# Performance work log

Hardware: AMD Instinct MI355X
Metric: run time of the kernel (lower is better)

The kernel has to match this reference:

```python
import jax, jax.numpy as jnp
import numpy as np

NEG_SLOPE = 0.2  # LeakyReLU slope from the torch module


def setup_inputs() -> dict:
    key = jax.random.key(0)
    k1, k2, k3 = jax.random.split(key, 3)
    B, N, IN = 32, 512, 256
    H, D = 8, 32  # out_dim=256, concat=True -> head_dim = 256 // 8
    x = jax.random.normal(k1, (B, N, IN), dtype=jnp.float32)
    # nn.Linear(in_dim, H*D, bias=False).weight has shape (H*D, in_dim)
    W = jax.random.normal(k2, (H * D, IN), dtype=jnp.float32) * (1.0 / np.sqrt(IN))
    # xavier_uniform on (1, H, 2D)
    limit = float(np.sqrt(6.0 / (H + 2 * D)))
    attn = jax.random.uniform(k3, (1, H, 2 * D), dtype=jnp.float32, minval=-limit, maxval=limit)
    return {"x": x, "W": W, "attn": attn}


def reference(x, W, attn):
    # x: (B, N, IN); W: (H*D, IN); attn: (1, H, 2D)
    B, N, _ = x.shape
    H = attn.shape[1]
    D = attn.shape[2] // 2
    Wx = (x @ W.T).reshape(B, N, H, D)  # (B, N, H, D)
    # Additive attention decomposes: e[b,i,j,h] = leaky(s_src[b,i,h] + s_tgt[b,j,h]).
    # (src = Wx broadcast over j, tgt = Wx broadcast over i; cat*attn sums split in two.)
    a_src = attn[0, :, :D]  # (H, D)
    a_tgt = attn[0, :, D:]  # (H, D)
    s_src = jnp.einsum('bnhd,hd->bnh', Wx, a_src)
    s_tgt = jnp.einsum('bnhd,hd->bnh', Wx, a_tgt)
    e = jax.nn.leaky_relu(s_src[:, :, None, :] + s_tgt[:, None, :, :], NEG_SLOPE)  # (B,N,N,H)
    a = jax.nn.softmax(e, axis=2)  # softmax over source nodes j
    # dropout p=0 (eval mode) -> identity
    out = jnp.einsum('bijh,bjhd->bihd', a, Wx)  # (B, N, H, D)
    out = out.reshape(B, N, H * D)  # concat=True
    return jax.nn.elu(out)
```

## Files before the change

kernel.cpp:

```cpp
#include <hip/hip_runtime.h>
#include <math.h>

#define NEG_SLOPE 0.2f
#define LOG2E 1.44269504088896f

typedef _Float16 f16x8 __attribute__((ext_vector_type(8)));
typedef float f32x4 __attribute__((ext_vector_type(4)));

union PK8 { uint4 u4; _Float16 h[8]; };
union PK4 { uint2 u2; _Float16 h[4]; };
union PK1 { unsigned short u; _Float16 h; };

__global__ __launch_bounds__(256) void gemm_wxt(const float* __restrict__ x,
                                                const float* __restrict__ W,
                                                unsigned short* __restrict__ wxtg) {
    __shared__ __align__(16) unsigned short xs[64 * 64];
    __shared__ __align__(16) unsigned short pool[128 * 64];
    unsigned short* ws = pool;
    unsigned short* tb = pool;

    const int tid = threadIdx.x;
    const int bid = blockIdx.x;
    const int m0 = (bid >> 1) * 64;
    const int n0 = (bid & 1) * 128;
    const int w = tid >> 6, l = tid & 63;
    const int q = l >> 4, ln = l & 15;
    const int iw = (w & 1) * 32, nw = (w >> 1) * 64;

    f32x4 acc[2][4];
    #pragma unroll
    for (int g = 0; g < 2; ++g)
        #pragma unroll
        for (int t = 0; t < 4; ++t) acc[g][t] = (f32x4){0.f, 0.f, 0.f, 0.f};

    for (int kc = 0; kc < 256; kc += 64) {
        __syncthreads();
        {
            const int i = tid >> 2, kq = tid & 3;
            const float* src = x + (size_t)(m0 + i) * 256 + kc + kq * 16;
            float4 v0 = *(const float4*)(src + 0);
            float4 v1 = *(const float4*)(src + 4);
            float4 v2 = *(const float4*)(src + 8);
            float4 v3 = *(const float4*)(src + 12);
            PK8 p0, p1;
            p0.h[0] = (_Float16)v0.x; p0.h[1] = (_Float16)v0.y;
            p0.h[2] = (_Float16)v0.z; p0.h[3] = (_Float16)v0.w;
            p0.h[4] = (_Float16)v1.x; p0.h[5] = (_Float16)v1.y;
            p0.h[6] = (_Float16)v1.z; p0.h[7] = (_Float16)v1.w;
            p1.h[0] = (_Float16)v2.x; p1.h[1] = (_Float16)v2.y;
            p1.h[2] = (_Float16)v2.z; p1.h[3] = (_Float16)v2.w;
            p1.h[4] = (_Float16)v3.x; p1.h[5] = (_Float16)v3.y;
            p1.h[6] = (_Float16)v3.z; p1.h[7] = (_Float16)v3.w;
            int b0 = i * 128 + kq * 32;
            *(uint4*)((char*)xs + (b0 ^ ((i & 7) << 4))) = p0.u4;
            *(uint4*)((char*)xs + ((b0 + 16) ^ ((i & 7) << 4))) = p1.u4;
        }
        {
            const int kq = tid & 15, nr = tid >> 4;
            #pragma unroll
            for (int p = 0; p < 8; ++p) {
                int n = p * 16 + nr;
                float4 v = *(const float4*)(W + (size_t)(n0 + n) * 256 + kc + kq * 4);
                PK4 pk;
                pk.h[0] = (_Float16)v.x; pk.h[1] = (_Float16)v.y;
                pk.h[2] = (_Float16)v.z; pk.h[3] = (_Float16)v.w;
                *(uint2*)((char*)ws + ((n * 128 + kq * 8) ^ ((n & 7) << 4))) = pk.u2;
            }
        }
        __syncthreads();

        #pragma unroll
        for (int ks = 0; ks < 2; ++ks) {
            const int kb = ks * 64 + q * 16;
            f16x8 af[2];
            #pragma unroll
            for (int g = 0; g < 2; ++g) {
                int row = iw + g * 16 + ln;
                uint4 raw = *(const uint4*)((const char*)xs +
                            ((row * 128 + kb) ^ ((row & 7) << 4)));
                PK8 pk; pk.u4 = raw;
                af[g] = *(f16x8*)&pk;
            }
            #pragma unroll
            for (int t = 0; t < 4; ++t) {
                int n = nw + t * 16 + ln;
                uint4 raw = *(const uint4*)((const char*)ws +
                            ((n * 128 + kb) ^ ((n & 7) << 4)));
                PK8 pk; pk.u4 = raw;
                f16x8 bf = *(f16x8*)&pk;
                acc[0][t] = __builtin_amdgcn_mfma_f32_16x16x32_f16(af[0], bf, acc[0][t], 0, 0, 0);
                acc[1][t] = __builtin_amdgcn_mfma_f32_16x16x32_f16(af[1], bf, acc[1][t], 0, 0, 0);
            }
        }
    }

    __syncthreads();
    #pragma unroll
    for (int g = 0; g < 2; ++g)
        #pragma unroll
        for (int t = 0; t < 4; ++t)
            #pragma unroll
            for (int r = 0; r < 4; ++r) {
                int n  = nw + t * 16 + ln;
                int jl = iw + g * 16 + q * 4 + r;
                PK1 hv; hv.h = (_Float16)acc[g][t][r];
                *(unsigned short*)((char*)tb + ((n * 128 + jl * 2) ^ ((n & 7) << 4))) = hv.u;
            }
    __syncthreads();
    {
        const int b = m0 >> 9, j0 = m0 & 511;
        #pragma unroll
        for (int p = 0; p < 4; ++p) {
            int idx = p * 256 + tid;
            int n = idx >> 3, c = idx & 7;
            uint4 v = *(const uint4*)((const char*)tb + ((n * 128 + c * 16) ^ ((n & 7) << 4)));
            int nn = n0 + n;
            *(uint4*)(wxtg + ((size_t)(b * 256 + nn) * 512 + j0 + c * 8)) = v;
        }
    }
}

__global__ __launch_bounds__(512) void gat_attn(const unsigned short* __restrict__ wxtg,
                                                const float* __restrict__ attn,
                                                float* __restrict__ out) {
    __shared__ __align__(16) unsigned short wxt[32 * 512];
    __shared__ float stf[512];
    __shared__ float ssrc[512];
    __shared__ float red_s[8];

    const int bid = blockIdx.x;
    const int bh = bid & 255, q4 = bid >> 8;
    const int b = bh >> 3, h = bh & 7;
    const int tid = threadIdx.x;
    const int w = tid >> 6, l = tid & 63;
    const int q = l >> 4, ln = l & 15;

    {
        const unsigned short* src = wxtg + (size_t)bh * 32 * 512;
        const int d = tid >> 4, cs = tid & 15;
        #pragma unroll
        for (int p = 0; p < 4; ++p) {
            int c = p * 16 + cs;
            uint4 v = *(const uint4*)(src + d * 512 + c * 8);
            *(uint4*)((char*)wxt + ((d * 1024 + c * 16) ^ ((d & 7) << 4))) = v;
        }
    }
    __syncthreads();

    {
        const int j = tid;
        float ss = 0.f, st = 0.f;
        #pragma unroll
        for (int d = 0; d < 32; ++d) {
            PK1 hv;
            hv.u = *(const unsigned short*)((const char*)wxt +
                    ((d * 1024 + j * 2) ^ ((d & 7) << 4)));
            float v = (float)hv.h;
            ss += v * attn[h * 64 + d];
            st += v * attn[h * 64 + 32 + d];
        }
        ssrc[j] = ss * LOG2E;
        float stv = st * LOG2E;
        stf[j] = stv;
        float m = stv;
        #pragma unroll
        for (int off = 32; off > 0; off >>= 1)
            m = fmaxf(m, __shfl_xor(m, off));
        if (l == 0) red_s[w] = m;
    }
    __syncthreads();
    float maxtK = red_s[0];
    #pragma unroll
    for (int ww = 1; ww < 8; ++ww) maxtK = fmaxf(maxtK, red_s[ww]);

    const int ibase = q4 * 128 + w * 16;
    float ciK, miK;
    {
        float cc = ssrc[ibase + ln];
        float cm = cc + maxtK;
        miK = fmaxf(cm, NEG_SLOPE * cm);
        ciK = cc;
    }

    f32x4 acc0 = (f32x4){0.f, 0.f, 0.f, 0.f};
    f32x4 acc1 = (f32x4){0.f, 0.f, 0.f, 0.f};
    float pd = 0.f;

    for (int kk = 0; kk < 16; ++kk) {
        const int j0 = kk * 32 + q * 8;
        float4 s0 = *(const float4*)(stf + j0);
        float4 s1 = *(const float4*)(stf + j0 + 4);
        float st[8] = {s0.x, s0.y, s0.z, s0.w, s1.x, s1.y, s1.z, s1.w};

        f16x8 bf[2];
        #pragma unroll
        for (int dt = 0; dt < 2; ++dt) {
            int d = dt * 16 + ln;
            int bb = d * 1024 + kk * 64 + q * 16;
            uint4 raw = *(const uint4*)((const char*)wxt + (bb ^ ((d & 7) << 4)));
            PK8 pk; pk.u4 = raw;
            bf[dt] = *(f16x8*)&pk;
        }

        f16x8 pa;
        float s = 0.f;
        #pragma unroll
        for (int e = 0; e < 8; ++e) {
            float eK = ciK + st[e];
            float lr = fmaxf(eK, NEG_SLOPE * eK);
            float p = exp2f(lr - miK);
            s += p;
            pa[e] = (_Float16)p;
        }
        pd += s;
        acc0 = __builtin_amdgcn_mfma_f32_16x16x32_f16(pa, bf[0], acc0, 0, 0, 0);
        acc1 = __builtin_amdgcn_mfma_f32_16x16x32_f16(pa, bf[1], acc1, 0, 0, 0);
    }

    pd += __shfl_xor(pd, 16);
    pd += __shfl_xor(pd, 32);
    float inv = 1.f / pd;

    #pragma unroll
    for (int dt = 0; dt < 2; ++dt) {
        f32x4 a = dt ? acc1 : acc0;
        #pragma unroll
        for (int r = 0; r < 4; ++r) {
            int row = q * 4 + r;
            float dn = __shfl(inv, row);
            float o = a[r] * dn;
            o = o > 0.f ? o : (__expf(o) - 1.f);
            size_t i = (size_t)(b * 512 + ibase + row);
            out[i * 256 + h * 32 + dt * 16 + ln] = o;
        }
    }
}

extern "C" void kernel_launch(void* const* d_in, const int* in_sizes, int n_in,
                              void* d_out, int out_size, void* d_ws, size_t ws_size,
                              hipStream_t stream) {
    const float* x    = (const float*)d_in[0];
    const float* W    = (const float*)d_in[1];
    const float* attn = (const float*)d_in[2];
    float* out = (float*)d_out;

    unsigned short* wxtg = (unsigned short*)d_ws;

    gemm_wxt<<<512, 256, 0, stream>>>(x, W, wxtg);
    gat_attn<<<1024, 512, 0, stream>>>(wxtg, attn, out);
}
```

Before: 44.52 us.

## Pre-convert inputs to fp16, halve attention grid with two row groups per warp

Adds a separate kernel that converts x and W to fp16 in workspace, so the GEMM loads half-width data and W is no longer converted again by every block. The attention kernel now handles 32 rows per warp (two MFMA row groups) over 512 blocks instead of 1024. This halves the redundant per-block staging of Wx and the score computation, and it switches to the hardware exp2 builtin. The cost is an extra launch plus a full fp16 round trip of x through global memory, and fewer blocks with more registers per thread.

Result: faster. 39.24 us (-11.9%).

```diff
diff --git a/kernel.cpp b/kernel.cpp
--- a/kernel.cpp
+++ b/kernel.cpp
@@ -4,15 +4,49 @@
 #define NEG_SLOPE 0.2f
 #define LOG2E 1.44269504088896f
 
+#if __has_builtin(__builtin_amdgcn_exp2f)
+#define EXP2F __builtin_amdgcn_exp2f
+#else
+#define EXP2F exp2f
+#endif
+
 typedef _Float16 f16x8 __attribute__((ext_vector_type(8)));
 typedef float f32x4 __attribute__((ext_vector_type(4)));
 
 union PK8 { uint4 u4; _Float16 h[8]; };
-union PK4 { uint2 u2; _Float16 h[4]; };
 union PK1 { unsigned short u; _Float16 h; };
 
-__global__ __launch_bounds__(256) void gemm_wxt(const float* __restrict__ x,
-                                                const float* __restrict__ W,
+#define XN_CHUNKS (32 * 512 * 256 / 8)
+#define WN_CHUNKS (256 * 256 / 8)
+
+__global__ __launch_bounds__(256) void cvt_f16(const float* __restrict__ x,
+                                               const float* __restrict__ W,
+                                               unsigned short* __restrict__ xf,
+                                               unsigned short* __restrict__ wf) {
+    int idx = blockIdx.x * 256 + threadIdx.x;
+    const float* src;
+    unsigned short* dst;
+    if (idx < XN_CHUNKS) {
+        src = x + (size_t)idx * 8;
+        dst = xf + (size_t)idx * 8;
+    } else {
+        int j = idx - XN_CHUNKS;
+        if (j >= WN_CHUNKS) return;
+        src = W + (size_t)j * 8;
+        dst = wf + (size_t)j * 8;
+    }
+    float4 v0 = *(const float4*)(src);
+    float4 v1 = *(const float4*)(src + 4);
+    PK8 p;
+    p.h[0] = (_Float16)v0.x; p.h[1] = (_Float16)v0.y;
+    p.h[2] = (_Float16)v0.z; p.h[3] = (_Float16)v0.w;
+    p.h[4] = (_Float16)v1.x; p.h[5] = (_Float16)v1.y;
+    p.h[6] = (_Float16)v1.z; p.h[7] = (_Float16)v1.w;
+    *(uint4*)dst = p.u4;
+}
+
+__global__ __launch_bounds__(256) void gemm_wxt(const unsigned short* __restrict__ xf,
+                                                const unsigned short* __restrict__ wf,
                                                 unsigned short* __restrict__ wxtg) {
     __shared__ __align__(16) unsigned short xs[64 * 64];
     __shared__ __align__(16) unsigned short pool[128 * 64];
@@ -35,37 +69,19 @@
 
     for (int kc = 0; kc < 256; kc += 64) {
         __syncthreads();
-        {
-            const int i = tid >> 2, kq = tid & 3;
-            const float* src = x + (size_t)(m0 + i) * 256 + kc + kq * 16;
-            float4 v0 = *(const float4*)(src + 0);
-            float4 v1 = *(const float4*)(src + 4);
-            float4 v2 = *(const float4*)(src + 8);
-            float4 v3 = *(const float4*)(src + 12);
-            PK8 p0, p1;
-            p0.h[0] = (_Float16)v0.x; p0.h[1] = (_Float16)v0.y;
-            p0.h[2] = (_Float16)v0.z; p0.h[3] = (_Float16)v0.w;
-            p0.h[4] = (_Float16)v1.x; p0.h[5] = (_Float16)v1.y;
-            p0.h[6] = (_Float16)v1.z; p0.h[7] = (_Float16)v1.w;
-            p1.h[0] = (_Float16)v2.x; p1.h[1] = (_Float16)v2.y;
-            p1.h[2] = (_Float16)v2.z; p1.h[3] = (_Float16)v2.w;
-            p1.h[4] = (_Float16)v3.x; p1.h[5] = (_Float16)v3.y;
-            p1.h[6] = (_Float16)v3.z; p1.h[7] = (_Float16)v3.w;
-            int b0 = i * 128 + kq * 32;
-            *(uint4*)((char*)xs + (b0 ^ ((i & 7) << 4))) = p0.u4;
-            *(uint4*)((char*)xs + ((b0 + 16) ^ ((i & 7) << 4))) = p1.u4;
-        }
-        {
-            const int kq = tid & 15, nr = tid >> 4;
-            #pragma unroll
-            for (int p = 0; p < 8; ++p) {
-                int n = p * 16 + nr;
-                float4 v = *(const float4*)(W + (size_t)(n0 + n) * 256 + kc + kq * 4);
-                PK4 pk;
-                pk.h[0] = (_Float16)v.x; pk.h[1] = (_Float16)v.y;
-                pk.h[2] = (_Float16)v.z; pk.h[3] = (_Float16)v.w;
-                *(uint2*)((char*)ws + ((n * 128 + kq * 8) ^ ((n & 7) << 4))) = pk.u2;
-            }
+        #pragma unroll
+        for (int p = 0; p < 2; ++p) {
+            int idx = p * 256 + tid;
+            int row = idx >> 3, c = idx & 7;
+            uint4 v = *(const uint4*)(xf + (size_t)(m0 + row) * 256 + kc + c * 8);
+            *(uint4*)((char*)xs + ((row * 128 + c * 16) ^ ((row & 7) << 4))) = v;
+        }
+        #pragma unroll
+        for (int p = 0; p < 4; ++p) {
+            int idx = p * 256 + tid;
+            int n = idx >> 3, c = idx & 7;
+            uint4 v = *(const uint4*)(wf + (size_t)(n0 + n) * 256 + kc + c * 8);
+            *(uint4*)((char*)ws + ((n * 128 + c * 16) ^ ((n & 7) << 4))) = v;
         }
         __syncthreads();
 
@@ -120,16 +136,16 @@
     }
 }
 
-__global__ __launch_bounds__(512) void gat_attn(const unsigned short* __restrict__ wxtg,
-                                                const float* __restrict__ attn,
-                                                float* __restrict__ out) {
+__global__ __launch_bounds__(512, 4) void gat_attn(const unsigned short* __restrict__ wxtg,
+                                                   const float* __restrict__ attn,
+                                                   float* __restrict__ out) {
     __shared__ __align__(16) unsigned short wxt[32 * 512];
     __shared__ float stf[512];
     __shared__ float ssrc[512];
     __shared__ float red_s[8];
 
     const int bid = blockIdx.x;
-    const int bh = bid & 255, q4 = bid >> 8;
+    const int bh = bid & 255, half = bid >> 8;
     const int b = bh >> 3, h = bh & 7;
     const int tid = threadIdx.x;
     const int w = tid >> 6, l = tid & 63;
@@ -173,18 +189,23 @@
     #pragma unroll
     for (int ww = 1; ww < 8; ++ww) maxtK = fmaxf(maxtK, red_s[ww]);
 
-    const int ibase = q4 * 128 + w * 16;
-    float ciK, miK;
-    {
-        float cc = ssrc[ibase + ln];
+    const int ibase = half * 256 + w * 32;
+    float ciK[2], miK[2];
+    #pragma unroll
+    for (int g = 0; g < 2; ++g) {
+        float cc = ssrc[ibase + g * 16 + ln];
         float cm = cc + maxtK;
-        miK = fmaxf(cm, NEG_SLOPE * cm);
-        ciK = cc;
-    }
-
-    f32x4 acc0 = (f32x4){0.f, 0.f, 0.f, 0.f};
-    f32x4 acc1 = (f32x4){0.f, 0.f, 0.f, 0.f};
-    float pd = 0.f;
+        miK[g] = fmaxf(cm, NEG_SLOPE * cm);
+        ciK[g] = cc;
+    }
+
+    f32x4 acc[2][2];
+    #pragma unroll
+    for (int g = 0; g < 2; ++g) {
+        acc[g][0] = (f32x4){0.f, 0.f, 0.f, 0.f};
+        acc[g][1] = (f32x4){0.f, 0.f, 0.f, 0.f};
+    }
+    float pd[2] = {0.f, 0.f};
 
     for (int kk = 0; kk < 16; ++kk) {
         const int j0 = kk * 32 + q * 8;
@@ -202,38 +223,45 @@
             bf[dt] = *(f16x8*)&pk;
         }
 
-        f16x8 pa;
-        float s = 0.f;
-        #pragma unroll
-        for (int e = 0; e < 8; ++e) {
-            float eK = ciK + st[e];
-            float lr = fmaxf(eK, NEG_SLOPE * eK);
-            float p = exp2f(lr - miK);
-            s += p;
-            pa[e] = (_Float16)p;
-        }
-        pd += s;
-        acc0 = __builtin_amdgcn_mfma_f32_16x16x32_f16(pa, bf[0], acc0, 0, 0, 0);
-        acc1 = __builtin_amdgcn_mfma_f32_16x16x32_f16(pa, bf[1], acc1, 0, 0, 0);
-    }
-
-    pd += __shfl_xor(pd, 16);
-    pd += __shfl_xor(pd, 32);
-    float inv = 1.f / pd;
-
-    #pragma unroll
-    for (int dt = 0; dt < 2; ++dt) {
-        f32x4 a = dt ? acc1 : acc0;
-        #pragma unroll
-        for (int r = 0; r < 4; ++r) {
-            int row = q * 4 + r;
-            float dn = __shfl(inv, row);
-            float o = a[r] * dn;
-            o = o > 0.f ? o : (__expf(o) - 1.f);
-            size_t i = (size_t)(b * 512 + ibase + row);
-            out[i * 256 + h * 32 + dt * 16 + ln] = o;
-        }
-    }
+        #pragma unroll
+        for (int g = 0; g < 2; ++g) {
+            f16x8 pa;
+            float s = 0.f;
+            #pragma unroll
+            for (int e = 0; e < 8; ++e) {
+                float eK = ciK[g] + st[e];
+                float lr = fmaxf(eK, NEG_SLOPE * eK);
+                float p = EXP2F(lr - miK[g]);
+                s += p;
+                pa[e] = (_Float16)p;
+            }
+            pd[g] += s;
+            acc[g][0] = __builtin_amdgcn_mfma_f32_16x16x32_f16(pa, bf[0], acc[g][0], 0, 0, 0);
+            acc[g][1] = __builtin_amdgcn_mfma_f32_16x16x32_f16(pa, bf[1], acc[g][1], 0, 0, 0);
+        }
+    }
+
+    float inv[2];
+    #pragma unroll
+    for (int g = 0; g < 2; ++g) {
+        float s = pd[g];
+        s += __shfl_xor(s, 16);
+        s += __shfl_xor(s, 32);
+        inv[g] = 1.f / s;
+    }
+    #pragma unroll
+    for (int g = 0; g < 2; ++g)
+        #pragma unroll
+        for (int dt = 0; dt < 2; ++dt)
+            #pragma unroll
+            for (int r = 0; r < 4; ++r) {
+                int row = q * 4 + r;
+                float dn = __shfl(inv[g], row);
+                float o = acc[g][dt][r] * dn;
+                o = o > 0.f ? o : (__expf(o) - 1.f);
+                size_t i = (size_t)(b * 512 + ibase + g * 16 + row);
+                out[i * 256 + h * 32 + dt * 16 + ln] = o;
+            }
 }
 
 extern "C" void kernel_launch(void* const* d_in, const int* in_sizes, int n_in,
@@ -244,8 +272,11 @@
     const float* attn = (const float*)d_in[2];
     float* out = (float*)d_out;
 
-    unsigned short* wxtg = (unsigned short*)d_ws;
-
-    gemm_wxt<<<512, 256, 0, stream>>>(x, W, wxtg);
-    gat_attn<<<1024, 512, 0, stream>>>(wxtg, attn, out);
-}
+    unsigned short* xf   = (unsigned short*)d_ws;
+    unsigned short* wf   = xf + (size_t)32 * 512 * 256;
+    unsigned short* wxtg = wf + 256 * 256;
+
+    cvt_f16<<<(XN_CHUNKS + WN_CHUNKS + 255) / 256, 256, 0, stream>>>(x, W, xf, wf);
+    gemm_wxt<<<512, 256, 0, stream>>>(xf, wf, wxtg);
+    gat_attn<<<512, 512, 0, stream>>>(wxtg, attn, out);
+}
```
